# Kernel optimization log

Measured on AMD Instinct MI355X. Metric: run time of the kernel, lower is better.

## Reference

```python
import jax, jax.numpy as jnp
import numpy as np

TEMPERATURE = 0.07
EPS = 1e-12  # F.normalize eps


def _l2_normalize(x):
    # matches torch F.normalize(dim=1): x / max(||x||, eps)
    n = jnp.linalg.norm(x, axis=1, keepdims=True)
    return x / jnp.maximum(n, EPS)


def setup_inputs() -> dict:
    key = jax.random.key(0)
    k1, k2 = jax.random.split(key)
    N, Z = 4096, 256
    z1 = jax.random.normal(k1, (N, Z), dtype=jnp.float32)
    z2 = jax.random.normal(k2, (N, Z), dtype=jnp.float32)
    return {"z1": z1, "z2": z2}


def reference(z1, z2):
    N = z1.shape[0]
    z1n = _l2_normalize(z1)
    z2n = _l2_normalize(z2)
    reps = jnp.concatenate([z1n, z2n], axis=0)          # [2N, Z]
    sim = reps @ reps.T                                  # cosine sim (rows unit-norm)
    # positives: sim[i, i+N] for i<N and sim[i, i-N] for i>=N
    pos = jnp.concatenate([jnp.diagonal(sim, offset=N),
                           jnp.diagonal(sim, offset=-N)])  # [2N]
    # The row logits are {positive} U {all sims except self and positive},
    # i.e. all entries except the self-similarity diagonal.
    inv_t = 1.0 / TEMPERATURE
    twoN = 2 * N
    diag_mask = jnp.eye(twoN, dtype=bool)
    logits = jnp.where(diag_mask, -jnp.inf, sim * inv_t)   # [2N, 2N]
    lse = jax.nn.logsumexp(logits, axis=1)                 # [2N]
    # cross_entropy with label at the positive: -pos/T + lse, sum / 2N
    loss = jnp.mean(lse - pos * inv_t)
    return loss
```

## Files before the change

kernel.cpp:

```cpp
#include <hip/hip_runtime.h>
#include <hip/hip_bf16.h>

#define N_ROWS 4096
#define TWO_N  8192
#define ZDIM   256
#define INV_T  (1.0f/0.07f)
#define EXP_SCALE (INV_T * 1.44269504088896340736f)

typedef __attribute__((ext_vector_type(4))) float f32x4;

__device__ __forceinline__ void async_load16(const void* g, void* lds_uniform_base) {
  __builtin_amdgcn_global_load_lds(
      (const __attribute__((address_space(1))) void*)g,
      (__attribute__((address_space(3))) void*)lds_uniform_base, 16, 0, 0);
}

__device__ __forceinline__ unsigned char f32_to_e4m3(float x) {
  unsigned int u = __float_as_uint(x);
  const unsigned int s = u >> 31;
  unsigned int a = u & 0x7FFFFFFFu;
  if (a > 0x43E00000u) a = 0x43E00000u;
  const float f = __uint_as_float(a);
  unsigned int out;
  if (a < (121u << 23)) {
    const int m = (int)rintf(f * 512.0f);
    out = (unsigned int)m;
  } else {
    const unsigned int r = a + 0x7FFFFu + ((a >> 20) & 1u);
    const unsigned int e8 = (r >> 23) - 120u;
    out = (e8 << 3) | ((r >> 20) & 7u);
  }
  return (unsigned char)(out | (s << 7));
}

__global__ __launch_bounds__(256) void normalize_kernel(
    const float* __restrict__ z1, const float* __restrict__ z2,
    unsigned char* __restrict__ reps, float* __restrict__ pos,
    float* __restrict__ out) {
  const int lane = threadIdx.x & 63;
  const int wave = threadIdx.x >> 6;
  const int r = blockIdx.x * 4 + wave;
  const float4 a = ((const float4*)(z1 + (size_t)r * ZDIM))[lane];
  const float4 b = ((const float4*)(z2 + (size_t)r * ZDIM))[lane];
  float s1 = a.x*a.x + a.y*a.y + a.z*a.z + a.w*a.w;
  float s2 = b.x*b.x + b.y*b.y + b.z*b.z + b.w*b.w;
  float s3 = a.x*b.x + a.y*b.y + a.z*b.z + a.w*b.w;
  #pragma unroll
  for (int m = 1; m < 64; m <<= 1) {
    s1 += __shfl_xor(s1, m, 64);
    s2 += __shfl_xor(s2, m, 64);
    s3 += __shfl_xor(s3, m, 64);
  }
  const float inv1 = 1.0f / fmaxf(sqrtf(s1), 1e-12f);
  const float inv2 = 1.0f / fmaxf(sqrtf(s2), 1e-12f);
  uchar4 pa, pb;
  pa.x = f32_to_e4m3(a.x * inv1); pa.y = f32_to_e4m3(a.y * inv1);
  pa.z = f32_to_e4m3(a.z * inv1); pa.w = f32_to_e4m3(a.w * inv1);
  pb.x = f32_to_e4m3(b.x * inv2); pb.y = f32_to_e4m3(b.y * inv2);
  pb.z = f32_to_e4m3(b.z * inv2); pb.w = f32_to_e4m3(b.w * inv2);
  ((uchar4*)(reps + (size_t)r * ZDIM))[lane] = pa;
  ((uchar4*)(reps + (size_t)(r + N_ROWS) * ZDIM))[lane] = pb;
  if (lane == 0) {
    pos[r] = s3 * inv1 * inv2;
    if (r == 0) out[0] = INV_T;
  }
}

__global__ __launch_bounds__(256, 2) void simsum_kernel(
    const unsigned char* __restrict__ reps,
    float* __restrict__ rowscratch,
    float* __restrict__ colscratch) {
  __shared__ __align__(16) unsigned char Alds[128 * 256];
  __shared__ __align__(16) unsigned char Blds[2][128 * 128];
  __shared__ float colred[2][256];

  const int tid  = threadIdx.x;
  const int lane = tid & 63;
  const int wave = tid >> 6;
  const int wm = wave >> 1, wn = wave & 1;
  const int quad = lane >> 4;
  const int l16  = lane & 15;
  const int itile = blockIdx.x;
  const int chunk = blockIdx.y;
  const int rowBase = itile * 128;
  const char* gbase = (const char*)reps;
  const bool diaghere = (chunk == 0);

  {
    const int r0 = tid >> 4;
    const int src = (tid & 8) | ((tid ^ (tid >> 4)) & 7);
    const char* g0 = gbase + (rowBase + r0) * ZDIM + src * 16;
    char* l0 = (char*)Alds + (wave << 10);
    #pragma unroll
    for (int p = 0; p < 8; ++p)
      async_load16(g0 + p * 16 * ZDIM, l0 + p * 4096);
  }

  int doff[4];
  int noff;
  if (diaghere) {
    doff[0] = 1; doff[1] = 2; doff[2] = 3; doff[3] = 32;
    noff = (itile < 32) ? 4 : 3;
  } else {
    doff[0] = chunk * 4; doff[1] = chunk * 4 + 1;
    doff[2] = chunk * 4 + 2; doff[3] = chunk * 4 + 3;
    noff = 4;
  }
  const int Q = noff * 2;

#define STAGE_B(q_) do {                                                        \
    const int t_ = (q_) >> 1, c_ = (q_) & 1;                                    \
    const int jt_ = (itile + doff[t_]) & 63;                                    \
    const int r0_ = tid >> 3;                                        \
    const int src_ = (tid ^ (tid >> 3)) & 7;                                    \
    const char* g0_ = gbase + (jt_ * 128 + r0_) * ZDIM + c_ * 128 + src_ * 16;  \
    char* l0_ = (char*)Blds[c_] + (wave << 10);                                 \
    _Pragma("unroll")                                                           \
    for (int p_ = 0; p_ < 4; ++p_)                                              \
      async_load16(g0_ + p_ * 32 * ZDIM, l0_ + p_ * 4096);                      \
  } while (0)

  float rowpart[16];
  #pragma unroll
  for (int i = 0; i < 16; ++i) rowpart[i] = 0.0f;
  const f32x4 zero4 = {0.0f, 0.0f, 0.0f, 0.0f};

  if (diaghere) {
    __syncthreads();
    if (Q > 0) STAGE_B(0);
    f32x4 acc[4][4];
    #pragma unroll
    for (int mi = 0; mi < 4; ++mi)
      #pragma unroll
      for (int ni = 0; ni < 4; ++ni) acc[mi][ni] = zero4;
    #pragma unroll
    for (int w = 0; w < 8; ++w) {
      const int o = w * 4 + quad;
      const int k16 = o >> 1, half = (o & 1) * 8;
      long afrag[4], bfrag[4];
      #pragma unroll
      for (int mi = 0; mi < 4; ++mi) {
        const int m = wm * 64 + mi * 16 + l16;
        const int sw = (k16 & 8) | ((k16 ^ m) & 7);
        afrag[mi] = *(const long*)((const char*)Alds + m * 256 + sw * 16 + half);
      }
      #pragma unroll
      for (int ni = 0; ni < 4; ++ni) {
        const int n = wn * 64 + ni * 16 + l16;
        const int sw = (k16 & 8) | ((k16 ^ n) & 7);
        bfrag[ni] = *(const long*)((const char*)Alds + n * 256 + sw * 16 + half);
      }
      #pragma unroll
      for (int mi = 0; mi < 4; ++mi)
        #pragma unroll
        for (int ni = 0; ni < 4; ++ni)
          acc[mi][ni] = __builtin_amdgcn_mfma_f32_16x16x32_fp8_fp8(
              afrag[mi], bfrag[ni], acc[mi][ni], 0, 0, 0);
    }
    #pragma unroll
    for (int mi = 0; mi < 4; ++mi)
      #pragma unroll
      for (int r = 0; r < 4; ++r) {
        const int grow = rowBase + wm * 64 + mi * 16 + quad * 4 + r;
        float s = 0.0f;
        #pragma unroll
        for (int ni = 0; ni < 4; ++ni) {
          const int gcol = rowBase + wn * 64 + ni * 16 + l16;
          const float e = exp2f((acc[mi][ni][r] - 1.0f) * EXP_SCALE);
          if (grow != gcol) s += e;
        }
        rowpart[mi * 4 + r] += s;
      }
    __syncthreads();
  } else {
    STAGE_B(0);
    __syncthreads();
  }

  f32x4 acc[4][4];
  for (int q = 0; q < Q; ++q) {
    if (q + 1 < Q) STAGE_B(q + 1);
    const int t = q >> 1, c = q & 1;
    const int d = doff[t];
    const int jtile = (itile + d) & 63;
    const int colBase = jtile * 128;

    if (c == 0) {
      #pragma unroll
      for (int mi = 0; mi < 4; ++mi)
        #pragma unroll
        for (int ni = 0; ni < 4; ++ni) acc[mi][ni] = zero4;
    }
    #pragma unroll
    for (int ws = 0; ws < 4; ++ws) {
      const int o  = c * 16 + ws * 4 + quad;
      const int k16 = o >> 1, half = (o & 1) * 8;
      const int ol = ws * 4 + quad;
      const int k16l = ol >> 1, halfl = (ol & 1) * 8;
      long afrag[4], bfrag[4];
      #pragma unroll
      for (int mi = 0; mi < 4; ++mi) {
        const int m = wm * 64 + mi * 16 + l16;
        const int sw = (k16 & 8) | ((k16 ^ m) & 7);
        afrag[mi] = *(const long*)((const char*)Alds + m * 256 + sw * 16 + half);
      }
      #pragma unroll
      for (int ni = 0; ni < 4; ++ni) {
        const int n = wn * 64 + ni * 16 + l16;
        const int sw = (k16l ^ n) & 7;
        bfrag[ni] = *(const long*)((const char*)Blds[c] + n * 128 + sw * 16 + halfl);
      }
      #pragma unroll
      for (int mi = 0; mi < 4; ++mi)
        #pragma unroll
        for (int ni = 0; ni < 4; ++ni)
          acc[mi][ni] = __builtin_amdgcn_mfma_f32_16x16x32_fp8_fp8(
              afrag[mi], bfrag[ni], acc[mi][ni], 0, 0, 0);
    }

    if (c == 1) {
      float colpart[4] = {0.0f, 0.0f, 0.0f, 0.0f};
      #pragma unroll
      for (int mi = 0; mi < 4; ++mi)
        #pragma unroll
        for (int r = 0; r < 4; ++r) {
          float s = 0.0f;
          #pragma unroll
          for (int ni = 0; ni < 4; ++ni) {
            const float e = exp2f((acc[mi][ni][r] - 1.0f) * EXP_SCALE);
            s += e;
            colpart[ni] += e;
          }
          rowpart[mi * 4 + r] += s;
        }
      #pragma unroll
      for (int ni = 0; ni < 4; ++ni) {
        float v = colpart[ni];
        v += __shfl_xor(v, 16, 64);
        v += __shfl_xor(v, 32, 64);
        if (quad == 0) colred[t & 1][wm * 128 + wn * 64 + ni * 16 + l16] = v;
      }
      __syncthreads();
      if (tid < 128)
        colscratch[(jtile * 32 + (d - 1)) * 128 + tid] =
            colred[t & 1][tid] + colred[t & 1][128 + tid];
    } else {
      __syncthreads();
    }
  }

  #pragma unroll
  for (int i = 0; i < 16; ++i) {
    float v = rowpart[i];
    v += __shfl_xor(v, 1, 64);
    v += __shfl_xor(v, 2, 64);
    v += __shfl_xor(v, 4, 64);
    v += __shfl_xor(v, 8, 64);
    rowpart[i] = v;
  }
  __syncthreads();
  if (l16 == 0) {
    #pragma unroll
    for (int mi = 0; mi < 4; ++mi)
      #pragma unroll
      for (int r = 0; r < 4; ++r)
        colred[0][wn * 128 + wm * 64 + mi * 16 + quad * 4 + r] = rowpart[mi * 4 + r];
  }
  __syncthreads();
  if (tid < 128)
    rowscratch[(itile * 8 + chunk) * 128 + tid] = colred[0][tid] + colred[0][128 + tid];
#undef STAGE_B
}

__global__ __launch_bounds__(256) void reduce_kernel(
    const float* __restrict__ rowscratch, const float* __restrict__ colscratch,
    const float* __restrict__ pos, float* __restrict__ out) {
  const int j = blockIdx.x;
  const int tid = threadIdx.x;
  float v = 0.0f;
  if (tid < 128) {
    float s = 0.0f;
    #pragma unroll
    for (int c = 0; c < 8; ++c) s += rowscratch[(j * 8 + c) * 128 + tid];
    const int ns = (j < 32) ? 31 : 32;
    for (int si = 0; si < ns; ++si) s += colscratch[(j * 32 + si) * 128 + tid];
    v = logf(s) * (1.0f / (float)TWO_N);
  } else if (tid < 192) {
    v = -pos[j * 64 + (tid - 128)] * (INV_T / (float)N_ROWS);
  }
  #pragma unroll
  for (int m = 1; m < 64; m <<= 1) v += __shfl_xor(v, m, 64);
  __shared__ float red[4];
  if ((tid & 63) == 0) red[tid >> 6] = v;
  __syncthreads();
  if (tid == 0) atomicAdd(out, red[0] + red[1] + red[2] + red[3]);
}

extern "C" void kernel_launch(void* const* d_in, const int* in_sizes, int n_in,
                              void* d_out, int out_size, void* d_ws, size_t ws_size,
                              hipStream_t stream) {
  const float* z1 = (const float*)d_in[0];
  const float* z2 = (const float*)d_in[1];
  char* ws = (char*)d_ws;
  unsigned char* reps = (unsigned char*)ws;
  size_t off = (size_t)TWO_N * ZDIM;
  float* pos = (float*)(ws + off);        off += N_ROWS * 4;
  float* rowscratch = (float*)(ws + off); off += 64 * 8 * 128 * 4;
  float* colscratch = (float*)(ws + off); off += 64 * 32 * 128 * 4;

  normalize_kernel<<<1024, 256, 0, stream>>>(z1, z2, reps, pos, (float*)d_out);
  simsum_kernel<<<dim3(64, 8), 256, 0, stream>>>(reps, rowscratch, colscratch);
  reduce_kernel<<<64, 256, 0, stream>>>(rowscratch, colscratch, pos, (float*)d_out);
}
```

Baseline: 95.85 us.

## Load B fragments directly from global into registers, drop LDS staging and barriers

Instead of staging each B tile into shared memory with async global-to-LDS copies and barriers, each wave loads its MFMA B fragments straight from global memory into registers, double-buffered across K halves. The diagonal tile is folded into the same loop with a masking flag. Per-wave partial row and column sums are written directly to scratch without a shared-memory reduction, so the scratch buffers double in size and the reduce kernel sums twice as many entries. This removes most __syncthreads and LDS traffic but relies on uncoalesced 8-byte global loads and more registers.

After: 110.5 us. 1.15x slower.

```diff
diff --git a/kernel.cpp b/kernel.cpp
--- a/kernel.cpp
+++ b/kernel.cpp
@@ -71,8 +71,6 @@
     float* __restrict__ rowscratch,
     float* __restrict__ colscratch) {
   __shared__ __align__(16) unsigned char Alds[128 * 256];
-  __shared__ __align__(16) unsigned char Blds[2][128 * 128];
-  __shared__ float colred[2][256];
 
   const int tid  = threadIdx.x;
   const int lane = tid & 63;
@@ -84,7 +82,6 @@
   const int chunk = blockIdx.y;
   const int rowBase = itile * 128;
   const char* gbase = (const char*)reps;
-  const bool diaghere = (chunk == 0);
 
   {
     const int r0 = tid >> 4;
@@ -96,28 +93,50 @@
       async_load16(g0 + p * 16 * ZDIM, l0 + p * 4096);
   }
 
-  int doff[4];
-  int noff;
-  if (diaghere) {
-    doff[0] = 1; doff[1] = 2; doff[2] = 3; doff[3] = 32;
-    noff = (itile < 32) ? 4 : 3;
+  int doff[5];
+  int nd;
+  if (chunk == 0) {
+    doff[0] = 0; doff[1] = 1; doff[2] = 2; doff[3] = 3; doff[4] = 32;
+    nd = (itile < 32) ? 5 : 4;
   } else {
     doff[0] = chunk * 4; doff[1] = chunk * 4 + 1;
     doff[2] = chunk * 4 + 2; doff[3] = chunk * 4 + 3;
-    noff = 4;
-  }
-  const int Q = noff * 2;
-
-#define STAGE_B(q_) do {                                                        \
+    doff[4] = 0;
+    nd = 4;
+  }
+  const int Q = nd * 2;
+
+#define PREF(q_, buf_) do {                                                     \
     const int t_ = (q_) >> 1, c_ = (q_) & 1;                                    \
     const int jt_ = (itile + doff[t_]) & 63;                                    \
-    const int r0_ = tid >> 3;                                        \
-    const int src_ = (tid ^ (tid >> 3)) & 7;                                    \
-    const char* g0_ = gbase + (jt_ * 128 + r0_) * ZDIM + c_ * 128 + src_ * 16;  \
-    char* l0_ = (char*)Blds[c_] + (wave << 10);                                 \
+    const char* bp_ = gbase + (size_t)(jt_ * 128 + wn * 64 + l16) * ZDIM        \
+                      + c_ * 128 + quad * 8;                                    \
     _Pragma("unroll")                                                           \
-    for (int p_ = 0; p_ < 4; ++p_)                                              \
-      async_load16(g0_ + p_ * 32 * ZDIM, l0_ + p_ * 4096);                      \
+    for (int ni_ = 0; ni_ < 4; ++ni_)                                           \
+      _Pragma("unroll")                                                         \
+      for (int s_ = 0; s_ < 4; ++s_)                                            \
+        buf_[ni_ * 4 + s_] = *(const long*)(bp_ + ni_ * 16 * ZDIM + s_ * 32);   \
+  } while (0)
+
+#define KSTEPS(c_, buf_) do {                                                   \
+    _Pragma("unroll")                                                           \
+    for (int ws_ = 0; ws_ < 4; ++ws_) {                                         \
+      const int o_ = (c_) * 16 + ws_ * 4 + quad;                                \
+      const int k16_ = o_ >> 1, h_ = (o_ & 1) * 8;                              \
+      long afrag_[4];                                                           \
+      _Pragma("unroll")                                                         \
+      for (int mi_ = 0; mi_ < 4; ++mi_) {                                       \
+        const int m_ = wm * 64 + mi_ * 16 + l16;                                \
+        const int sw_ = (k16_ & 8) | ((k16_ ^ m_) & 7);                         \
+        afrag_[mi_] = *(const long*)((const char*)Alds + m_ * 256 + sw_ * 16 + h_); \
+      }                                                                         \
+      _Pragma("unroll")                                                         \
+      for (int mi_ = 0; mi_ < 4; ++mi_)                                         \
+        _Pragma("unroll")                                                       \
+        for (int ni_ = 0; ni_ < 4; ++ni_)                                       \
+          acc[mi_][ni_] = __builtin_amdgcn_mfma_f32_16x16x32_fp8_fp8(           \
+              afrag_[mi_], buf_[ni_ * 4 + ws_], acc[mi_][ni_], 0, 0, 0);        \
+    }                                                                           \
   } while (0)
 
   float rowpart[16];
@@ -125,38 +144,28 @@
   for (int i = 0; i < 16; ++i) rowpart[i] = 0.0f;
   const f32x4 zero4 = {0.0f, 0.0f, 0.0f, 0.0f};
 
-  if (diaghere) {
-    __syncthreads();
-    if (Q > 0) STAGE_B(0);
-    f32x4 acc[4][4];
+  long b0[16], b1[16];
+  f32x4 acc[4][4];
+
+  PREF(0, b0);
+  __syncthreads();
+
+  for (int q = 0; q < Q; q += 2) {
+    if (q + 1 < Q) PREF(q + 1, b1);
     #pragma unroll
     for (int mi = 0; mi < 4; ++mi)
       #pragma unroll
       for (int ni = 0; ni < 4; ++ni) acc[mi][ni] = zero4;
-    #pragma unroll
-    for (int w = 0; w < 8; ++w) {
-      const int o = w * 4 + quad;
-      const int k16 = o >> 1, half = (o & 1) * 8;
-      long afrag[4], bfrag[4];
-      #pragma unroll
-      for (int mi = 0; mi < 4; ++mi) {
-        const int m = wm * 64 + mi * 16 + l16;
-        const int sw = (k16 & 8) | ((k16 ^ m) & 7);
-        afrag[mi] = *(const long*)((const char*)Alds + m * 256 + sw * 16 + half);
-      }
-      #pragma unroll
-      for (int ni = 0; ni < 4; ++ni) {
-        const int n = wn * 64 + ni * 16 + l16;
-        const int sw = (k16 & 8) | ((k16 ^ n) & 7);
-        bfrag[ni] = *(const long*)((const char*)Alds + n * 256 + sw * 16 + half);
-      }
-      #pragma unroll
-      for (int mi = 0; mi < 4; ++mi)
-        #pragma unroll
-        for (int ni = 0; ni < 4; ++ni)
-          acc[mi][ni] = __builtin_amdgcn_mfma_f32_16x16x32_fp8_fp8(
-              afrag[mi], bfrag[ni], acc[mi][ni], 0, 0, 0);
-    }
+    KSTEPS(0, b0);
+
+    if (q + 2 < Q) PREF(q + 2, b0);
+    KSTEPS(1, b1);
+
+    const int t = q >> 1;
+    const int d = doff[t];
+    const int jtile = (itile + d) & 63;
+    const bool diag = (d == 0);
+    float colpart[4] = {0.0f, 0.0f, 0.0f, 0.0f};
     #pragma unroll
     for (int mi = 0; mi < 4; ++mi)
       #pragma unroll
@@ -165,89 +174,26 @@
         float s = 0.0f;
         #pragma unroll
         for (int ni = 0; ni < 4; ++ni) {
-          const int gcol = rowBase + wn * 64 + ni * 16 + l16;
+          const int gcol = jtile * 128 + wn * 64 + ni * 16 + l16;
           const float e = exp2f((acc[mi][ni][r] - 1.0f) * EXP_SCALE);
-          if (grow != gcol) s += e;
+          if (!diag || grow != gcol) s += e;
+          colpart[ni] += e;
         }
         rowpart[mi * 4 + r] += s;
       }
-    __syncthreads();
-  } else {
-    STAGE_B(0);
-    __syncthreads();
-  }
-
-  f32x4 acc[4][4];
-  for (int q = 0; q < Q; ++q) {
-    if (q + 1 < Q) STAGE_B(q + 1);
-    const int t = q >> 1, c = q & 1;
-    const int d = doff[t];
-    const int jtile = (itile + d) & 63;
-    const int colBase = jtile * 128;
-
-    if (c == 0) {
-      #pragma unroll
-      for (int mi = 0; mi < 4; ++mi)
-        #pragma unroll
-        for (int ni = 0; ni < 4; ++ni) acc[mi][ni] = zero4;
-    }
-    #pragma unroll
-    for (int ws = 0; ws < 4; ++ws) {
-      const int o  = c * 16 + ws * 4 + quad;
-      const int k16 = o >> 1, half = (o & 1) * 8;
-      const int ol = ws * 4 + quad;
-      const int k16l = ol >> 1, halfl = (ol & 1) * 8;
-      long afrag[4], bfrag[4];
-      #pragma unroll
-      for (int mi = 0; mi < 4; ++mi) {
-        const int m = wm * 64 + mi * 16 + l16;
-        const int sw = (k16 & 8) | ((k16 ^ m) & 7);
-        afrag[mi] = *(const long*)((const char*)Alds + m * 256 + sw * 16 + half);
-      }
-      #pragma unroll
-      for (int ni = 0; ni < 4; ++ni) {
-        const int n = wn * 64 + ni * 16 + l16;
-        const int sw = (k16l ^ n) & 7;
-        bfrag[ni] = *(const long*)((const char*)Blds[c] + n * 128 + sw * 16 + halfl);
-      }
-      #pragma unroll
-      for (int mi = 0; mi < 4; ++mi)
-        #pragma unroll
-        for (int ni = 0; ni < 4; ++ni)
-          acc[mi][ni] = __builtin_amdgcn_mfma_f32_16x16x32_fp8_fp8(
-              afrag[mi], bfrag[ni], acc[mi][ni], 0, 0, 0);
-    }
-
-    if (c == 1) {
-      float colpart[4] = {0.0f, 0.0f, 0.0f, 0.0f};
-      #pragma unroll
-      for (int mi = 0; mi < 4; ++mi)
-        #pragma unroll
-        for (int r = 0; r < 4; ++r) {
-          float s = 0.0f;
-          #pragma unroll
-          for (int ni = 0; ni < 4; ++ni) {
-            const float e = exp2f((acc[mi][ni][r] - 1.0f) * EXP_SCALE);
-            s += e;
-            colpart[ni] += e;
-          }
-          rowpart[mi * 4 + r] += s;
-        }
+    if (!diag) {
       #pragma unroll
       for (int ni = 0; ni < 4; ++ni) {
         float v = colpart[ni];
         v += __shfl_xor(v, 16, 64);
         v += __shfl_xor(v, 32, 64);
-        if (quad == 0) colred[t & 1][wm * 128 + wn * 64 + ni * 16 + l16] = v;
+        if (quad == 0)
+          colscratch[(((jtile * 32) + (d - 1)) * 2 + wm) * 128 + wn * 64 + ni * 16 + l16] = v;
       }
-      __syncthreads();
-      if (tid < 128)
-        colscratch[(jtile * 32 + (d - 1)) * 128 + tid] =
-            colred[t & 1][tid] + colred[t & 1][128 + tid];
-    } else {
-      __syncthreads();
     }
   }
+#undef PREF
+#undef KSTEPS
 
   #pragma unroll
   for (int i = 0; i < 16; ++i) {
@@ -258,18 +204,14 @@
     v += __shfl_xor(v, 8, 64);
     rowpart[i] = v;
   }
-  __syncthreads();
   if (l16 == 0) {
     #pragma unroll
     for (int mi = 0; mi < 4; ++mi)
       #pragma unroll
       for (int r = 0; r < 4; ++r)
-        colred[0][wn * 128 + wm * 64 + mi * 16 + quad * 4 + r] = rowpart[mi * 4 + r];
-  }
-  __syncthreads();
-  if (tid < 128)
-    rowscratch[(itile * 8 + chunk) * 128 + tid] = colred[0][tid] + colred[0][128 + tid];
-#undef STAGE_B
+        rowscratch[((itile * 8 + chunk) * 2 + wn) * 128 + wm * 64 + mi * 16 + quad * 4 + r]
+            = rowpart[mi * 4 + r];
+  }
 }
 
 __global__ __launch_bounds__(256) void reduce_kernel(
@@ -281,9 +223,15 @@
   if (tid < 128) {
     float s = 0.0f;
     #pragma unroll
-    for (int c = 0; c < 8; ++c) s += rowscratch[(j * 8 + c) * 128 + tid];
+    for (int c = 0; c < 8; ++c)
+      #pragma unroll
+      for (int w = 0; w < 2; ++w)
+        s += rowscratch[((j * 8 + c) * 2 + w) * 128 + tid];
     const int ns = (j < 32) ? 31 : 32;
-    for (int si = 0; si < ns; ++si) s += colscratch[(j * 32 + si) * 128 + tid];
+    for (int si = 0; si < ns; ++si)
+      #pragma unroll
+      for (int w = 0; w < 2; ++w)
+        s += colscratch[((j * 32 + si) * 2 + w) * 128 + tid];
     v = logf(s) * (1.0f / (float)TWO_N);
   } else if (tid < 192) {
     v = -pos[j * 64 + (tid - 128)] * (INV_T / (float)N_ROWS);
@@ -305,8 +253,8 @@
   unsigned char* reps = (unsigned char*)ws;
   size_t off = (size_t)TWO_N * ZDIM;
   float* pos = (float*)(ws + off);        off += N_ROWS * 4;
-  float* rowscratch = (float*)(ws + off); off += 64 * 8 * 128 * 4;
-  float* colscratch = (float*)(ws + off); off += 64 * 32 * 128 * 4;
+  float* rowscratch = (float*)(ws + off); off += 64 * 8 * 2 * 128 * 4;
+  float* colscratch = (float*)(ws + off); off += 64 * 32 * 2 * 128 * 4;
 
   normalize_kernel<<<1024, 256, 0, stream>>>(z1, z2, reps, pos, (float*)d_out);
   simsum_kernel<<<dim3(64, 8), 256, 0, stream>>>(reps, rowscratch, colscratch);
```

## Double simsum grid, drop LDS reductions, write per-wave partials to scratch

Applied to the files above, without the earlier changes.

The similarity kernel's grid doubles from 8 to 16 chunks per row tile, so each block handles 2 column tiles instead of 4, giving more blocks for the GPU's CUs. The LDS colred buffer and its block-level reductions are removed; each wave writes its row and column partial sums straight to larger scratch arrays, and the reduce kernel folds in the extra wave dimension. The exp shift by -1 is dropped, with the output initialised to 0 instead of INV_T to match. This trades fewer barriers and better occupancy for more scratch traffic, reloading the A tile in twice as many blocks, and a heavier reduce pass.

Result: no change. 96.64 us (+0.8%).

```diff
diff --git a/kernel.cpp b/kernel.cpp
--- a/kernel.cpp
+++ b/kernel.cpp
@@ -62,7 +62,7 @@
   ((uchar4*)(reps + (size_t)(r + N_ROWS) * ZDIM))[lane] = pb;
   if (lane == 0) {
     pos[r] = s3 * inv1 * inv2;
-    if (r == 0) out[0] = INV_T;
+    if (r == 0) out[0] = 0.0f;
   }
 }
 
@@ -72,7 +72,6 @@
     float* __restrict__ colscratch) {
   __shared__ __align__(16) unsigned char Alds[128 * 256];
   __shared__ __align__(16) unsigned char Blds[2][128 * 128];
-  __shared__ float colred[2][256];
 
   const int tid  = threadIdx.x;
   const int lane = tid & 63;
@@ -96,25 +95,24 @@
       async_load16(g0 + p * 16 * ZDIM, l0 + p * 4096);
   }
 
-  int doff[4];
+  int doff[2];
   int noff;
   if (diaghere) {
-    doff[0] = 1; doff[1] = 2; doff[2] = 3; doff[3] = 32;
-    noff = (itile < 32) ? 4 : 3;
+    doff[0] = 1; doff[1] = 32;
+    noff = (itile < 32) ? 2 : 1;
   } else {
-    doff[0] = chunk * 4; doff[1] = chunk * 4 + 1;
-    doff[2] = chunk * 4 + 2; doff[3] = chunk * 4 + 3;
-    noff = 4;
+    doff[0] = 2 * chunk; doff[1] = 2 * chunk + 1;
+    noff = 2;
   }
   const int Q = noff * 2;
 
 #define STAGE_B(q_) do {                                                        \
     const int t_ = (q_) >> 1, c_ = (q_) & 1;                                    \
     const int jt_ = (itile + doff[t_]) & 63;                                    \
-    const int r0_ = tid >> 3;                                        \
+    const int r0_ = tid >> 3;                                                   \
     const int src_ = (tid ^ (tid >> 3)) & 7;                                    \
     const char* g0_ = gbase + (jt_ * 128 + r0_) * ZDIM + c_ * 128 + src_ * 16;  \
-    char* l0_ = (char*)Blds[c_] + (wave << 10);                                 \
+    char* l0_ = (char*)Blds[(q_) & 1] + (wave << 10);                           \
     _Pragma("unroll")                                                           \
     for (int p_ = 0; p_ < 4; ++p_)                                              \
       async_load16(g0_ + p_ * 32 * ZDIM, l0_ + p_ * 4096);                      \
@@ -166,7 +164,7 @@
         #pragma unroll
         for (int ni = 0; ni < 4; ++ni) {
           const int gcol = rowBase + wn * 64 + ni * 16 + l16;
-          const float e = exp2f((acc[mi][ni][r] - 1.0f) * EXP_SCALE);
+          const float e = exp2f(acc[mi][ni][r] * EXP_SCALE);
           if (grow != gcol) s += e;
         }
         rowpart[mi * 4 + r] += s;
@@ -183,7 +181,6 @@
     const int t = q >> 1, c = q & 1;
     const int d = doff[t];
     const int jtile = (itile + d) & 63;
-    const int colBase = jtile * 128;
 
     if (c == 0) {
       #pragma unroll
@@ -196,7 +193,7 @@
       const int o  = c * 16 + ws * 4 + quad;
       const int k16 = o >> 1, half = (o & 1) * 8;
       const int ol = ws * 4 + quad;
-      const int k16l = ol >> 1, halfl = (ol & 1) * 8;
+      const int sl = ol >> 1, halfl = (ol & 1) * 8;
       long afrag[4], bfrag[4];
       #pragma unroll
       for (int mi = 0; mi < 4; ++mi) {
@@ -207,7 +204,7 @@
       #pragma unroll
       for (int ni = 0; ni < 4; ++ni) {
         const int n = wn * 64 + ni * 16 + l16;
-        const int sw = (k16l ^ n) & 7;
+        const int sw = sl ^ (n & 7);
         bfrag[ni] = *(const long*)((const char*)Blds[c] + n * 128 + sw * 16 + halfl);
       }
       #pragma unroll
@@ -219,6 +216,7 @@
     }
 
     if (c == 1) {
+      const int dm1 = d - 1;
       float colpart[4] = {0.0f, 0.0f, 0.0f, 0.0f};
       #pragma unroll
       for (int mi = 0; mi < 4; ++mi)
@@ -227,7 +225,7 @@
           float s = 0.0f;
           #pragma unroll
           for (int ni = 0; ni < 4; ++ni) {
-            const float e = exp2f((acc[mi][ni][r] - 1.0f) * EXP_SCALE);
+            const float e = exp2f(acc[mi][ni][r] * EXP_SCALE);
             s += e;
             colpart[ni] += e;
           }
@@ -238,16 +236,13 @@
         float v = colpart[ni];
         v += __shfl_xor(v, 16, 64);
         v += __shfl_xor(v, 32, 64);
-        if (quad == 0) colred[t & 1][wm * 128 + wn * 64 + ni * 16 + l16] = v;
-      }
-      __syncthreads();
-      if (tid < 128)
-        colscratch[(jtile * 32 + (d - 1)) * 128 + tid] =
-            colred[t & 1][tid] + colred[t & 1][128 + tid];
-    } else {
-      __syncthreads();
+        if (quad == 0)
+          colscratch[((jtile * 32 + dm1) * 2 + wm) * 128 + wn * 64 + ni * 16 + l16] = v;
+      }
     }
-  }
+    __syncthreads();
+  }
+#undef STAGE_B
 
   #pragma unroll
   for (int i = 0; i < 16; ++i) {
@@ -258,18 +253,14 @@
     v += __shfl_xor(v, 8, 64);
     rowpart[i] = v;
   }
-  __syncthreads();
   if (l16 == 0) {
     #pragma unroll
     for (int mi = 0; mi < 4; ++mi)
       #pragma unroll
       for (int r = 0; r < 4; ++r)
-        colred[0][wn * 128 + wm * 64 + mi * 16 + quad * 4 + r] = rowpart[mi * 4 + r];
-  }
-  __syncthreads();
-  if (tid < 128)
-    rowscratch[(itile * 8 + chunk) * 128 + tid] = colred[0][tid] + colred[0][128 + tid];
-#undef STAGE_B
+        rowscratch[((itile * 16 + chunk) * 2 + wn) * 128 + wm * 64 + mi * 16 + quad * 4 + r]
+            = rowpart[mi * 4 + r];
+  }
 }
 
 __global__ __launch_bounds__(256) void reduce_kernel(
@@ -281,9 +272,15 @@
   if (tid < 128) {
     float s = 0.0f;
     #pragma unroll
-    for (int c = 0; c < 8; ++c) s += rowscratch[(j * 8 + c) * 128 + tid];
+    for (int c = 0; c < 16; ++c)
+      #pragma unroll
+      for (int w = 0; w < 2; ++w)
+        s += rowscratch[((j * 16 + c) * 2 + w) * 128 + tid];
     const int ns = (j < 32) ? 31 : 32;
-    for (int si = 0; si < ns; ++si) s += colscratch[(j * 32 + si) * 128 + tid];
+    for (int si = 0; si < ns; ++si)
+      #pragma unroll
+      for (int w = 0; w < 2; ++w)
+        s += colscratch[((j * 32 + si) * 2 + w) * 128 + tid];
     v = logf(s) * (1.0f / (float)TWO_N);
   } else if (tid < 192) {
     v = -pos[j * 64 + (tid - 128)] * (INV_T / (float)N_ROWS);
@@ -305,10 +302,10 @@
   unsigned char* reps = (unsigned char*)ws;
   size_t off = (size_t)TWO_N * ZDIM;
   float* pos = (float*)(ws + off);        off += N_ROWS * 4;
-  float* rowscratch = (float*)(ws + off); off += 64 * 8 * 128 * 4;
-  float* colscratch = (float*)(ws + off); off += 64 * 32 * 128 * 4;
+  float* rowscratch = (float*)(ws + off); off += 64 * 16 * 2 * 128 * 4;
+  float* colscratch = (float*)(ws + off); off += 64 * 32 * 2 * 128 * 4;
 
   normalize_kernel<<<1024, 256, 0, stream>>>(z1, z2, reps, pos, (float*)d_out);
-  simsum_kernel<<<dim3(64, 8), 256, 0, stream>>>(reps, rowscratch, colscratch);
+  simsum_kernel<<<dim3(64, 16), 256, 0, stream>>>(reps, rowscratch, colscratch);
   reduce_kernel<<<64, 256, 0, stream>>>(rowscratch, colscratch, pos, (float*)d_out);
 }
```
